# Optimization experiments

Measured on AMD Instinct MI355X. Metric: run time of the kernel, lower is better.

## Reference

```python
import jax, jax.numpy as jnp
import numpy as np

# Static configuration (from init_kwargs)
SPLIT_SEC = (128, 320, 320)   # (n_nucl_species..., n_up, n_dn)
N = sum(SPLIT_SEC)            # 768 particles
N_NUCL = sum(SPLIT_SEC[:-2])  # 128
N_DN = SPLIT_SEC[-1]          # 320
SINGLE = 256
PAIR = 64
D_FEAT = SINGLE + len(SPLIT_SEC) * PAIR + len(SPLIT_SEC) * SINGLE  # 1216
SQRT2 = 1.4142135623730951
GELU_RESCALE = 1.7128586      # fvmc rescaled-gelu constant (unit output variance)

_SPLIT_IDX = np.cumsum(SPLIT_SEC)[:-1]

def _pair_type():
    pt = np.zeros((N, N), np.int32)
    sn, se = slice(0, N_NUCL), slice(N_NUCL, N)
    su = slice(N_NUCL, N_NUCL + SPLIT_SEC[-2])
    sd = slice(N_NUCL + SPLIT_SEC[-2], N)
    pt[sn, se] = pt[se, sn] = 1
    pt[su, su] = pt[sd, sd] = 2
    pt[su, sd] = pt[sd, su] = 3
    return pt

PAIR_TYPE = _pair_type()  # static int mask, values in {0,1,2,3}

def actv(x):
    # parse_activation('gelu', rescale=True)
    return jax.nn.gelu(x) * GELU_RESCALE

def residual(x, y):
    # adaptive_residual with rescale=True (shapes always match here)
    return (x + y) / SQRT2

def aggregate_features(h1, h2):
    # per-section mean of h1 over particles -> (n_sec, d1), tiled to (N, n_sec, d1)
    h1_mean = jnp.stack([s.mean(axis=0) for s in jnp.split(h1, _SPLIT_IDX, axis=0)], axis=0)
    h1_mean = jnp.tile(h1_mean[None], (N, 1, 1))
    # per-section mean of h2 over axis 1 -> (N, n_sec, d2)
    h2_mean = jnp.stack([s.mean(axis=1) for s in jnp.split(h2, _SPLIT_IDX, axis=1)], axis=-2)
    # spin symmetry: swap the last two (up/dn) mean channels for the dn rows
    h1_sw = jnp.stack([h1_mean[-N_DN:, -1], h1_mean[-N_DN:, -2]], axis=1)
    h1_mean = h1_mean.at[-N_DN:, -2:].set(h1_sw)
    h2_sw = jnp.stack([h2_mean[-N_DN:, -1], h2_mean[-N_DN:, -2]], axis=1)
    h2_mean = h2_mean.at[-N_DN:, -2:].set(h2_sw)
    return jnp.concatenate([h1, h2_mean.reshape(N, -1), h1_mean.reshape(N, -1)], axis=-1)

def setup_inputs() -> dict:
    key = jax.random.key(0)
    ks = jax.random.split(key, 5)
    sc = lambda fan_in: 1.0 / np.sqrt(fan_in)  # lecun-normal-ish scale
    return {
        "h1": jax.random.normal(ks[0], (N, SINGLE), jnp.float32),
        "h2": jax.random.normal(ks[1], (N, N, PAIR), jnp.float32),
        "W1n": jax.random.normal(ks[2], (D_FEAT, SINGLE), jnp.float32) * sc(D_FEAT),
        "b1n": jnp.zeros((SINGLE,), jnp.float32),
        "W1e": jax.random.normal(ks[3], (D_FEAT, SINGLE), jnp.float32) * sc(D_FEAT),
        "b1e": jnp.zeros((SINGLE,), jnp.float32),
        "W2": jax.random.normal(ks[4], (4, PAIR, PAIR), jnp.float32) * sc(PAIR),
        "b2": jnp.zeros((4, PAIR), jnp.float32),
    }

def reference(h1, h2, W1n, b1n, W1e, b1e, W2, b2):
    feats = aggregate_features(h1, h2)  # (N, D_FEAT)
    # h1 update: separate Dense for nuclei vs electrons
    h1_new = jnp.concatenate([
        feats[:N_NUCL] @ W1n + b1n,
        feats[N_NUCL:] @ W1e + b1e,
    ], axis=0)
    h1_out = residual(h1, actv(h1_new))
    # h2 update: per pair-type Dense, masked scatter back (4 static types)
    pt = jnp.asarray(PAIR_TYPE)
    h2_new = jnp.zeros((N, N, PAIR), h2.dtype)
    for p in range(4):
        mask = (pt == p)[..., None]
        h2_new = h2_new + mask * (jnp.einsum('nmd,de->nme', h2, W2[p]) + b2[p])
    h2_out = residual(h2, actv(h2_new))
    return h1_out, h2_out
```

## Files before the change

### kernel.cpp

```cpp
#include <hip/hip_runtime.h>
#include <hip/hip_bf16.h>


#define NPART 768
#define NNUCL 128
#define H1OUT_ELEMS (768 * 256)

typedef short short8 __attribute__((ext_vector_type(8)));
typedef float f32x4 __attribute__((ext_vector_type(4)));

__device__ __forceinline__ unsigned short f2bf(float f) {
    unsigned u = __builtin_bit_cast(unsigned, f);
    unsigned r = u + 0x7fffu + ((u >> 16) & 1u);
    return (unsigned short)(r >> 16);
}

__device__ __forceinline__ float gelu_scaled(float x) {
    float y = 0.7978845608028654f * (x + 0.044715f * x * x * x);
    y = fminf(fmaxf(y, -15.f), 15.f);
    float e = __expf(2.f * y);
    float t = (e - 1.f) / (e + 1.f);
    return 0.5f * x * (1.f + t) * 1.7128586f;
}

__global__ __launch_bounds__(256) void k_h2(
    const float* __restrict__ h2, const float* __restrict__ W2,
    const float* __restrict__ b2, float* __restrict__ out2,
    float* __restrict__ part2 ) {
    const int ct = blockIdx.x;
    const int n  = blockIdx.y;
    const int m0 = ct * 64;

    const int rs = (n < 128) ? 0 : ((n < 448) ? 1 : 2);
    const int cs = (ct < 2) ? 0 : ((ct < 7) ? 1 : 2);
    int p;
    if (rs == 0)      p = (cs == 0) ? 0 : 1;
    else if (rs == 1) p = (cs == 0) ? 1 : ((cs == 1) ? 2 : 3);
    else              p = (cs == 0) ? 1 : ((cs == 1) ? 3 : 2);

    __shared__ float          A32[64][68];
    __shared__ unsigned short A16[64][72];
    __shared__ unsigned short BT[64][72];
    __shared__ float          red[4][64];

    const int t = threadIdx.x;

    const float* src = h2 + ((size_t)n * 768 + m0) * 64;
    #pragma unroll
    for (int i = 0; i < 4; ++i) {
        int f4 = i * 256 + t;
        int row = f4 >> 4;
        int c4 = (f4 & 15) << 2;
        float4 v = *reinterpret_cast<const float4*>(src + row * 64 + c4);
        *reinterpret_cast<float4*>(&A32[row][c4]) = v;
        ushort4 bv;
        bv.x = f2bf(v.x); bv.y = f2bf(v.y); bv.z = f2bf(v.z); bv.w = f2bf(v.w);
        *reinterpret_cast<ushort4*>(&A16[row][c4]) = bv;
    }
    const float* w = W2 + p * 4096;
    #pragma unroll
    for (int i = 0; i < 16; ++i) {
        int idx = i * 256 + t;
        int d = idx >> 6, e = idx & 63;
        BT[e][d] = f2bf(w[idx]);
    }
    __syncthreads();

    {
        int d = t & 63, mg = t >> 6;
        float s = 0.f;
        #pragma unroll
        for (int m = 0; m < 16; ++m) s += A32[mg * 16 + m][d];
        red[mg][d] = s;
    }
    __syncthreads();
    if (t < 64) {
        float s = red[0][t] + red[1][t] + red[2][t] + red[3][t];
        part2[((size_t)n * 12 + ct) * 64 + t] = s;
    }

    const int lane = t & 63;
    const int wv = t >> 6;
    const int wm = wv >> 1, we = wv & 1;
    const int lr = lane & 15;
    const int lk = lane >> 4;

    f32x4 acc[2][2] = {};
    #pragma unroll
    for (int kh = 0; kh < 2; ++kh) {
        short8 aF[2], bF[2];
        int k = kh * 32 + lk * 8;
        #pragma unroll
        for (int fm = 0; fm < 2; ++fm)
            aF[fm] = *reinterpret_cast<const short8*>(&A16[wm * 32 + fm * 16 + lr][k]);
        #pragma unroll
        for (int fe = 0; fe < 2; ++fe)
            bF[fe] = *reinterpret_cast<const short8*>(&BT[we * 32 + fe * 16 + lr][k]);
        #pragma unroll
        for (int fm = 0; fm < 2; ++fm)
            #pragma unroll
            for (int fe = 0; fe < 2; ++fe)
                acc[fm][fe] = __builtin_amdgcn_mfma_f32_16x16x32_bf16(
                    aF[fm], bF[fe], acc[fm][fe], 0, 0, 0);
    }

    float* dst = out2 + ((size_t)n * 768 + m0) * 64;
    #pragma unroll
    for (int fm = 0; fm < 2; ++fm) {
        #pragma unroll
        for (int fe = 0; fe < 2; ++fe) {
            int e = we * 32 + fe * 16 + lr;
            float bias = b2[p * 64 + e];
            #pragma unroll
            for (int r = 0; r < 4; ++r) {
                int m = wm * 32 + fm * 16 + lk * 4 + r;
                float x = acc[fm][fe][r] + bias;
                float g = gelu_scaled(x);
                dst[m * 64 + e] = (A32[m][e] + g) * 0.70710678118654752f;
            }
        }
    }
}

__global__ __launch_bounds__(256) void k_h1sum(const float* __restrict__ h1,
                                               float* __restrict__ part1) {
    int tile = blockIdx.x;
    int e = threadIdx.x;
    float s = 0.f;
    #pragma unroll 8
    for (int r = 0; r < 64; ++r) s += h1[(size_t)(tile * 64 + r) * 256 + e];
    part1[tile * 256 + e] = s;
}

__global__ __launch_bounds__(256) void k_wconv(
    const float* __restrict__ W1n, const float* __restrict__ W1e,
    unsigned short* __restrict__ WT) {
    const int k0 = blockIdx.x * 64;
    const int e0 = blockIdx.y * 64;
    const int mtx = blockIdx.z;
    const float* W = mtx ? W1e : W1n;
    __shared__ float tile[64][65];
    const int t = threadIdx.x;
    #pragma unroll
    for (int i = 0; i < 16; ++i) {
        int idx = i * 256 + t;
        int kr = idx >> 6, ec = idx & 63;
        tile[kr][ec] = W[(size_t)(k0 + kr) * 256 + e0 + ec];
    }
    __syncthreads();
    #pragma unroll
    for (int i = 0; i < 16; ++i) {
        int idx = i * 256 + t;
        int er = idx >> 6, kc = idx & 63;
        WT[((size_t)mtx * 256 + e0 + er) * 1216 + k0 + kc] = f2bf(tile[kc][er]);
    }
}

__global__ __launch_bounds__(256) void k_feats(
    const float* __restrict__ h1, const float* __restrict__ part2,
    const float* __restrict__ part1, unsigned short* __restrict__ feats) {
    const int n = blockIdx.x;
    const bool dnrow = (n >= 448);
    const int t = threadIdx.x;
    unsigned short* fr = feats + (size_t)n * 1216;

    fr[t] = f2bf(h1[(size_t)n * 256 + t]);

    if (t < 192) {
        int sec = t >> 6, d = t & 63;
        int s2 = (dnrow && sec >= 1) ? (3 - sec) : sec;
        const float* pr = part2 + (size_t)n * 768;
        float s;
        if (s2 == 0) {
            s = (pr[d] + pr[64 + d]) * (1.f / 128.f);
        } else if (s2 == 1) {
            s = 0.f;
            #pragma unroll
            for (int q = 2; q < 7; ++q) s += pr[q * 64 + d];
            s *= (1.f / 320.f);
        } else {
            s = 0.f;
            #pragma unroll
            for (int q = 7; q < 12; ++q) s += pr[q * 64 + d];
            s *= (1.f / 320.f);
        }
        fr[256 + t] = f2bf(s);
    }

    #pragma unroll
    for (int i = 0; i < 3; ++i) {
        int j = i * 256 + t;
        int sec = j >> 8, e2 = j & 255;
        int s2 = (dnrow && sec >= 1) ? (3 - sec) : sec;
        float s;
        if (s2 == 0) {
            s = (part1[e2] + part1[256 + e2]) * (1.f / 128.f);
        } else if (s2 == 1) {
            s = 0.f;
            #pragma unroll
            for (int q = 2; q < 7; ++q) s += part1[q * 256 + e2];
            s *= (1.f / 320.f);
        } else {
            s = 0.f;
            #pragma unroll
            for (int q = 7; q < 12; ++q) s += part1[q * 256 + e2];
            s *= (1.f / 320.f);
        }
        fr[448 + j] = f2bf(s);
    }
}

__global__ __launch_bounds__(256) void k_h1g(
    const unsigned short* __restrict__ feats, const unsigned short* __restrict__ WT,
    const float* __restrict__ b1n, const float* __restrict__ b1e,
    const float* __restrict__ h1, float* __restrict__ out1) {
    const int m0 = blockIdx.x * 16;
    const int wv = threadIdx.x >> 6;
    const int e0 = (blockIdx.y * 4 + wv) * 16;
    const int lane = threadIdx.x & 63;
    const int lr = lane & 15, lk = lane >> 4;
    const bool nucl = (m0 < NNUCL);
    const unsigned short* BT = WT + (nucl ? 0 : (size_t)256 * 1216);
    const float* bb = nucl ? b1n : b1e;

    const unsigned short* arow = feats + (size_t)(m0 + lr) * 1216 + lk * 8;
    const unsigned short* brow = BT + (size_t)(e0 + lr) * 1216 + lk * 8;

    f32x4 acc = {};
    #pragma unroll 2
    for (int k = 0; k < 1216; k += 32) {
        short8 aF = *reinterpret_cast<const short8*>(arow + k);
        short8 bF = *reinterpret_cast<const short8*>(brow + k);
        acc = __builtin_amdgcn_mfma_f32_16x16x32_bf16(aF, bF, acc, 0, 0, 0);
    }

    const int e = e0 + lr;
    const float bias = bb[e];
    #pragma unroll
    for (int r = 0; r < 4; ++r) {
        int m = m0 + lk * 4 + r;
        float x = acc[r] + bias;
        float g = gelu_scaled(x);
        out1[(size_t)m * 256 + e] =
            (h1[(size_t)m * 256 + e] + g) * 0.70710678118654752f;
    }
}

extern "C" void kernel_launch(void* const* d_in, const int* in_sizes, int n_in,
                              void* d_out, int out_size, void* d_ws, size_t ws_size,
                              hipStream_t stream) {
    const float* h1  = (const float*)d_in[0];
    const float* h2  = (const float*)d_in[1];
    const float* W1n = (const float*)d_in[2];
    const float* b1n = (const float*)d_in[3];
    const float* W1e = (const float*)d_in[4];
    const float* b1e = (const float*)d_in[5];
    const float* W2  = (const float*)d_in[6];
    const float* b2  = (const float*)d_in[7];

    float* out1 = (float*)d_out;
    float* out2 = out1 + H1OUT_ELEMS;

    float* part2 = (float*)d_ws;
    float* part1 = part2 + 768 * 12 * 64;
    unsigned short* feats = (unsigned short*)(part1 + 12 * 256);
    unsigned short* WT    = feats + (size_t)768 * 1216;

    k_h1sum<<<12, 256, 0, stream>>>(h1, part1);
    k_wconv<<<dim3(19, 4, 2), 256, 0, stream>>>(W1n, W1e, WT);
    k_h2<<<dim3(12, 768), 256, 0, stream>>>(h2, W2, b2, out2, part2);
    k_feats<<<768, 256, 0, stream>>>(h1, part2, part1, feats);
    k_h1g<<<dim3(48, 4), 256, 0, stream>>>(feats, WT, b1n, b1e, h1, out1);
}
```

Before: 86.55 us.

## Merge five kernels into two and streamline the h2 pass

Folds the h1 column-sum and the W1 transpose/convert kernels into the large h2 kernel as extra leading blocks, and merges the feature-assembly kernel into the h1 GEMM kernel, which now builds its feature rows in shared memory. The h2 path drops the fp32 shared-memory copy: column sums come from registers and the residual re-reads h2 from global, while outputs use nontemporal stores. GELU is rewritten as a sigmoid form using exp2 and rcp intrinsics with the residual folded in. The h1 GEMM computes two output tiles per wave. This cuts launch count and LDS traffic at the cost of a re-read of h2 and a slightly different GELU approximation.

```diff
diff --git a/kernel.cpp b/kernel.cpp
--- a/kernel.cpp
+++ b/kernel.cpp
@@ -1,9 +1,6 @@
 #include <hip/hip_runtime.h>
-#include <hip/hip_bf16.h>
-
-
-#define NPART 768
-#define NNUCL 128
+
+
 #define H1OUT_ELEMS (768 * 256)
 
 typedef short short8 __attribute__((ext_vector_type(8)));
@@ -15,20 +12,64 @@
     return (unsigned short)(r >> 16);
 }
 
-__device__ __forceinline__ float gelu_scaled(float x) {
-    float y = 0.7978845608028654f * (x + 0.044715f * x * x * x);
-    y = fminf(fmaxf(y, -15.f), 15.f);
-    float e = __expf(2.f * y);
-    float t = (e - 1.f) / (e + 1.f);
-    return 0.5f * x * (1.f + t) * 1.7128586f;
-}
-
-__global__ __launch_bounds__(256) void k_h2(
+__device__ __forceinline__ float gelu_res(float x, float hv) {
+    float x2 = x * x;
+    float z = x * fmaf(-0.1029432196f, x2, -2.3025850930f);
+    float e = __builtin_amdgcn_exp2f(z);
+    float r = __builtin_amdgcn_rcpf(1.f + e);
+    return fmaf(x * r, 1.2111740f, hv * 0.70710678f);
+}
+
+__global__ __launch_bounds__(256) void k_h2pre(
     const float* __restrict__ h2, const float* __restrict__ W2,
-    const float* __restrict__ b2, float* __restrict__ out2,
-    float* __restrict__ part2 ) {
-    const int ct = blockIdx.x;
-    const int n  = blockIdx.y;
+    const float* __restrict__ b2, const float* __restrict__ h1,
+    const float* __restrict__ W1n, const float* __restrict__ W1e,
+    float* __restrict__ out2, float* __restrict__ part2,
+    float* __restrict__ part1, unsigned short* __restrict__ WT) {
+    __shared__ union SM {
+        struct {
+            unsigned short A16[64][72];
+            unsigned short BT[64][72];
+            float          red[16][68];
+        } g;
+        float tile[64][65];
+    } sm;
+
+    int b = blockIdx.x;
+    const int t = threadIdx.x;
+
+    if (b < 12) {
+        float s = 0.f;
+        #pragma unroll 8
+        for (int r = 0; r < 64; ++r) s += h1[(size_t)(b * 64 + r) * 256 + t];
+        part1[b * 256 + t] = s;
+        return;
+    }
+    if (b < 164) {
+        int idx = b - 12;
+        int mtx = idx / 76;
+        int r2  = idx % 76;
+        int k0 = (r2 / 4) * 64, e0 = (r2 % 4) * 64;
+        const float* W = mtx ? W1e : W1n;
+        #pragma unroll
+        for (int i = 0; i < 16; ++i) {
+            int j = i * 256 + t;
+            int kr = j >> 6, ec = j & 63;
+            sm.tile[kr][ec] = W[(size_t)(k0 + kr) * 256 + e0 + ec];
+        }
+        __syncthreads();
+        #pragma unroll
+        for (int i = 0; i < 16; ++i) {
+            int j = i * 256 + t;
+            int er = j >> 6, kc = j & 63;
+            WT[((size_t)mtx * 256 + e0 + er) * 1216 + k0 + kc] = f2bf(sm.tile[kc][er]);
+        }
+        return;
+    }
+
+    b -= 164;
+    const int ct = b % 12;
+    const int n  = b / 12;
     const int m0 = ct * 64;
 
     const int rs = (n < 128) ? 0 : ((n < 448) ? 1 : 2);
@@ -38,49 +79,52 @@
     else if (rs == 1) p = (cs == 0) ? 1 : ((cs == 1) ? 2 : 3);
     else              p = (cs == 0) ? 1 : ((cs == 1) ? 3 : 2);
 
-    __shared__ float          A32[64][68];
-    __shared__ unsigned short A16[64][72];
-    __shared__ unsigned short BT[64][72];
-    __shared__ float          red[4][64];
-
-    const int t = threadIdx.x;
-
     const float* src = h2 + ((size_t)n * 768 + m0) * 64;
-    #pragma unroll
-    for (int i = 0; i < 4; ++i) {
-        int f4 = i * 256 + t;
-        int row = f4 >> 4;
-        int c4 = (f4 & 15) << 2;
-        float4 v = *reinterpret_cast<const float4*>(src + row * 64 + c4);
-        *reinterpret_cast<float4*>(&A32[row][c4]) = v;
+    const int row0 = t >> 4, c4 = (t & 15) << 2;
+
+    float4 v0 = *reinterpret_cast<const float4*>(src + (row0 +  0) * 64 + c4);
+    float4 v1 = *reinterpret_cast<const float4*>(src + (row0 + 16) * 64 + c4);
+    float4 v2 = *reinterpret_cast<const float4*>(src + (row0 + 32) * 64 + c4);
+    float4 v3 = *reinterpret_cast<const float4*>(src + (row0 + 48) * 64 + c4);
+
+    {
         ushort4 bv;
-        bv.x = f2bf(v.x); bv.y = f2bf(v.y); bv.z = f2bf(v.z); bv.w = f2bf(v.w);
-        *reinterpret_cast<ushort4*>(&A16[row][c4]) = bv;
+        bv.x = f2bf(v0.x); bv.y = f2bf(v0.y); bv.z = f2bf(v0.z); bv.w = f2bf(v0.w);
+        *reinterpret_cast<ushort4*>(&sm.g.A16[row0][c4]) = bv;
+        bv.x = f2bf(v1.x); bv.y = f2bf(v1.y); bv.z = f2bf(v1.z); bv.w = f2bf(v1.w);
+        *reinterpret_cast<ushort4*>(&sm.g.A16[row0 + 16][c4]) = bv;
+        bv.x = f2bf(v2.x); bv.y = f2bf(v2.y); bv.z = f2bf(v2.z); bv.w = f2bf(v2.w);
+        *reinterpret_cast<ushort4*>(&sm.g.A16[row0 + 32][c4]) = bv;
+        bv.x = f2bf(v3.x); bv.y = f2bf(v3.y); bv.z = f2bf(v3.z); bv.w = f2bf(v3.w);
+        *reinterpret_cast<ushort4*>(&sm.g.A16[row0 + 48][c4]) = bv;
+    }
+    {
+        float4 cs4;
+        cs4.x = v0.x + v1.x + v2.x + v3.x;
+        cs4.y = v0.y + v1.y + v2.y + v3.y;
+        cs4.z = v0.z + v1.z + v2.z + v3.z;
+        cs4.w = v0.w + v1.w + v2.w + v3.w;
+        *reinterpret_cast<float4*>(&sm.g.red[row0][c4]) = cs4;
     }
     const float* w = W2 + p * 4096;
     #pragma unroll
     for (int i = 0; i < 16; ++i) {
         int idx = i * 256 + t;
         int d = idx >> 6, e = idx & 63;
-        BT[e][d] = f2bf(w[idx]);
+        sm.g.BT[e][d] = f2bf(w[idx]);
     }
     __syncthreads();
-
-    {
-        int d = t & 63, mg = t >> 6;
-        float s = 0.f;
-        #pragma unroll
-        for (int m = 0; m < 16; ++m) s += A32[mg * 16 + m][d];
-        red[mg][d] = s;
-    }
-    __syncthreads();
-    if (t < 64) {
-        float s = red[0][t] + red[1][t] + red[2][t] + red[3][t];
-        part2[((size_t)n * 12 + ct) * 64 + t] = s;
-    }
 
     const int lane = t & 63;
     const int wv = t >> 6;
+
+    if (wv == 0) {
+        float s = 0.f;
+        #pragma unroll
+        for (int r = 0; r < 16; ++r) s += sm.g.red[r][lane];
+        part2[((size_t)n * 12 + ct) * 64 + lane] = s;
+    }
+
     const int wm = wv >> 1, we = wv & 1;
     const int lr = lane & 15;
     const int lk = lane >> 4;
@@ -92,10 +136,10 @@
         int k = kh * 32 + lk * 8;
         #pragma unroll
         for (int fm = 0; fm < 2; ++fm)
-            aF[fm] = *reinterpret_cast<const short8*>(&A16[wm * 32 + fm * 16 + lr][k]);
+            aF[fm] = *reinterpret_cast<const short8*>(&sm.g.A16[wm * 32 + fm * 16 + lr][k]);
         #pragma unroll
         for (int fe = 0; fe < 2; ++fe)
-            bF[fe] = *reinterpret_cast<const short8*>(&BT[we * 32 + fe * 16 + lr][k]);
+            bF[fe] = *reinterpret_cast<const short8*>(&sm.g.BT[we * 32 + fe * 16 + lr][k]);
         #pragma unroll
         for (int fm = 0; fm < 2; ++fm)
             #pragma unroll
@@ -114,135 +158,103 @@
             #pragma unroll
             for (int r = 0; r < 4; ++r) {
                 int m = wm * 32 + fm * 16 + lk * 4 + r;
-                float x = acc[fm][fe][r] + bias;
-                float g = gelu_scaled(x);
-                dst[m * 64 + e] = (A32[m][e] + g) * 0.70710678118654752f;
+                float hv = src[m * 64 + e];
+                float o = gelu_res(acc[fm][fe][r] + bias, hv);
+                __builtin_nontemporal_store(o, dst + m * 64 + e);
             }
         }
     }
 }
 
-__global__ __launch_bounds__(256) void k_h1sum(const float* __restrict__ h1,
-                                               float* __restrict__ part1) {
-    int tile = blockIdx.x;
-    int e = threadIdx.x;
-    float s = 0.f;
-    #pragma unroll 8
-    for (int r = 0; r < 64; ++r) s += h1[(size_t)(tile * 64 + r) * 256 + e];
-    part1[tile * 256 + e] = s;
-}
-
-__global__ __launch_bounds__(256) void k_wconv(
-    const float* __restrict__ W1n, const float* __restrict__ W1e,
-    unsigned short* __restrict__ WT) {
-    const int k0 = blockIdx.x * 64;
-    const int e0 = blockIdx.y * 64;
-    const int mtx = blockIdx.z;
-    const float* W = mtx ? W1e : W1n;
-    __shared__ float tile[64][65];
+__global__ __launch_bounds__(256) void k_h1f(
+    const float* __restrict__ h1, const unsigned short* __restrict__ WT,
+    const float* __restrict__ part2, const float* __restrict__ part1,
+    const float* __restrict__ b1n, const float* __restrict__ b1e,
+    float* __restrict__ out1) {
+    __shared__ unsigned short FL[16][1224];
+
+    const int n0 = blockIdx.x * 16;
+    const int half = blockIdx.y;
     const int t = threadIdx.x;
+    const bool dn = (n0 >= 448);
+    const bool nucl = (n0 < 128);
+
     #pragma unroll
     for (int i = 0; i < 16; ++i) {
         int idx = i * 256 + t;
-        int kr = idx >> 6, ec = idx & 63;
-        tile[kr][ec] = W[(size_t)(k0 + kr) * 256 + e0 + ec];
-    }
-    __syncthreads();
-    #pragma unroll
-    for (int i = 0; i < 16; ++i) {
+        int r = idx >> 8, c = idx & 255;
+        FL[r][c] = f2bf(h1[(size_t)(n0 + r) * 256 + c]);
+    }
+    #pragma unroll
+    for (int i = 0; i < 12; ++i) {
         int idx = i * 256 + t;
-        int er = idx >> 6, kc = idx & 63;
-        WT[((size_t)mtx * 256 + e0 + er) * 1216 + k0 + kc] = f2bf(tile[kc][er]);
-    }
-}
-
-__global__ __launch_bounds__(256) void k_feats(
-    const float* __restrict__ h1, const float* __restrict__ part2,
-    const float* __restrict__ part1, unsigned short* __restrict__ feats) {
-    const int n = blockIdx.x;
-    const bool dnrow = (n >= 448);
-    const int t = threadIdx.x;
-    unsigned short* fr = feats + (size_t)n * 1216;
-
-    fr[t] = f2bf(h1[(size_t)n * 256 + t]);
-
-    if (t < 192) {
-        int sec = t >> 6, d = t & 63;
-        int s2 = (dnrow && sec >= 1) ? (3 - sec) : sec;
-        const float* pr = part2 + (size_t)n * 768;
+        int r = idx / 192, c = idx % 192;
+        int sec = c >> 6, d = c & 63;
+        int s2 = (dn && sec >= 1) ? (3 - sec) : sec;
+        const float* pr = part2 + (size_t)(n0 + r) * 768;
         float s;
         if (s2 == 0) {
             s = (pr[d] + pr[64 + d]) * (1.f / 128.f);
-        } else if (s2 == 1) {
+        } else {
+            int q0 = (s2 == 1) ? 2 : 7;
             s = 0.f;
             #pragma unroll
-            for (int q = 2; q < 7; ++q) s += pr[q * 64 + d];
+            for (int q = 0; q < 5; ++q) s += pr[(q0 + q) * 64 + d];
             s *= (1.f / 320.f);
-        } else {
-            s = 0.f;
-            #pragma unroll
-            for (int q = 7; q < 12; ++q) s += pr[q * 64 + d];
-            s *= (1.f / 320.f);
-        }
-        fr[256 + t] = f2bf(s);
-    }
-
+        }
+        FL[r][256 + c] = f2bf(s);
+    }
     #pragma unroll
     for (int i = 0; i < 3; ++i) {
         int j = i * 256 + t;
         int sec = j >> 8, e2 = j & 255;
-        int s2 = (dnrow && sec >= 1) ? (3 - sec) : sec;
+        int s2 = (dn && sec >= 1) ? (3 - sec) : sec;
         float s;
         if (s2 == 0) {
             s = (part1[e2] + part1[256 + e2]) * (1.f / 128.f);
-        } else if (s2 == 1) {
+        } else {
+            int q0 = (s2 == 1) ? 2 : 7;
             s = 0.f;
             #pragma unroll
-            for (int q = 2; q < 7; ++q) s += part1[q * 256 + e2];
+            for (int q = 0; q < 5; ++q) s += part1[(q0 + q) * 256 + e2];
             s *= (1.f / 320.f);
-        } else {
-            s = 0.f;
-            #pragma unroll
-            for (int q = 7; q < 12; ++q) s += part1[q * 256 + e2];
-            s *= (1.f / 320.f);
-        }
-        fr[448 + j] = f2bf(s);
-    }
-}
-
-__global__ __launch_bounds__(256) void k_h1g(
-    const unsigned short* __restrict__ feats, const unsigned short* __restrict__ WT,
-    const float* __restrict__ b1n, const float* __restrict__ b1e,
-    const float* __restrict__ h1, float* __restrict__ out1) {
-    const int m0 = blockIdx.x * 16;
-    const int wv = threadIdx.x >> 6;
-    const int e0 = (blockIdx.y * 4 + wv) * 16;
-    const int lane = threadIdx.x & 63;
+        }
+        unsigned short bv = f2bf(s);
+        #pragma unroll
+        for (int r = 0; r < 16; ++r) FL[r][448 + j] = bv;
+    }
+    __syncthreads();
+
+    const int w = t >> 6, lane = t & 63;
     const int lr = lane & 15, lk = lane >> 4;
-    const bool nucl = (m0 < NNUCL);
+    const int e0 = half * 128 + w * 32;
     const unsigned short* BT = WT + (nucl ? 0 : (size_t)256 * 1216);
-    const float* bb = nucl ? b1n : b1e;
-
-    const unsigned short* arow = feats + (size_t)(m0 + lr) * 1216 + lk * 8;
-    const unsigned short* brow = BT + (size_t)(e0 + lr) * 1216 + lk * 8;
-
-    f32x4 acc = {};
+    const unsigned short* br0 = BT + (size_t)(e0 + lr) * 1216 + lk * 8;
+    const unsigned short* br1 = br0 + (size_t)16 * 1216;
+    const unsigned short* ar = &FL[lr][lk * 8];
+
+    f32x4 acc0 = {}, acc1 = {};
     #pragma unroll 2
     for (int k = 0; k < 1216; k += 32) {
-        short8 aF = *reinterpret_cast<const short8*>(arow + k);
-        short8 bF = *reinterpret_cast<const short8*>(brow + k);
-        acc = __builtin_amdgcn_mfma_f32_16x16x32_bf16(aF, bF, acc, 0, 0, 0);
-    }
-
-    const int e = e0 + lr;
-    const float bias = bb[e];
-    #pragma unroll
-    for (int r = 0; r < 4; ++r) {
-        int m = m0 + lk * 4 + r;
-        float x = acc[r] + bias;
-        float g = gelu_scaled(x);
-        out1[(size_t)m * 256 + e] =
-            (h1[(size_t)m * 256 + e] + g) * 0.70710678118654752f;
+        short8 aF = *reinterpret_cast<const short8*>(ar + k);
+        short8 b0 = *reinterpret_cast<const short8*>(br0 + k);
+        short8 b1 = *reinterpret_cast<const short8*>(br1 + k);
+        acc0 = __builtin_amdgcn_mfma_f32_16x16x32_bf16(aF, b0, acc0, 0, 0, 0);
+        acc1 = __builtin_amdgcn_mfma_f32_16x16x32_bf16(aF, b1, acc1, 0, 0, 0);
+    }
+
+    const float* bb = nucl ? b1n : b1e;
+    #pragma unroll
+    for (int j = 0; j < 2; ++j) {
+        const f32x4 a = j ? acc1 : acc0;
+        int e = e0 + j * 16 + lr;
+        float bias = bb[e];
+        #pragma unroll
+        for (int r = 0; r < 4; ++r) {
+            int m = n0 + lk * 4 + r;
+            float hv = h1[(size_t)m * 256 + e];
+            out1[(size_t)m * 256 + e] = gelu_res(a[r] + bias, hv);
+        }
     }
 }
 
@@ -263,12 +275,9 @@
 
     float* part2 = (float*)d_ws;
     float* part1 = part2 + 768 * 12 * 64;
-    unsigned short* feats = (unsigned short*)(part1 + 12 * 256);
-    unsigned short* WT    = feats + (size_t)768 * 1216;
-
-    k_h1sum<<<12, 256, 0, stream>>>(h1, part1);
-    k_wconv<<<dim3(19, 4, 2), 256, 0, stream>>>(W1n, W1e, WT);
-    k_h2<<<dim3(12, 768), 256, 0, stream>>>(h2, W2, b2, out2, part2);
-    k_feats<<<768, 256, 0, stream>>>(h1, part2, part1, feats);
-    k_h1g<<<dim3(48, 4), 256, 0, stream>>>(feats, WT, b1n, b1e, h1, out1);
-}
+    unsigned short* WT = (unsigned short*)(part1 + 12 * 256);
+
+    k_h2pre<<<dim3(164 + 12 * 768), 256, 0, stream>>>(
+        h2, W2, b2, h1, W1n, W1e, out2, part2, part1, WT);
+    k_h1f<<<dim3(48, 2), 256, 0, stream>>>(h1, WT, part2, part1, b1n, b1e, out1);
+}
```

Measured after the change: 86.28 us. Within noise of the previous version (-0.3%).
